# Kernel optimization log

Hardware: AMD Instinct MI355X
Metric: run time of the kernel (lower is better)

The kernel has to match this reference:

```python
import jax, jax.numpy as jnp
import numpy as np

B, N, H, HEADS, F, L = 32, 256, 512, 8, 2048, 8
D = H // HEADS  # per-head dim
EPS = 1e-5


def _layernorm(x, scale, bias):
    mu = jnp.mean(x, axis=-1, keepdims=True)
    var = jnp.mean(jnp.square(x - mu), axis=-1, keepdims=True)
    return (x - mu) * jax.lax.rsqrt(var + EPS) * scale + bias


def setup_inputs() -> dict:
    key = jax.random.key(0)
    ks = jax.random.split(key, 12)
    s = 0.02
    inp = {
        "x": jax.random.normal(ks[0], (B, N, H), jnp.float32),
        "attn_bias": jax.random.normal(ks[1], (B, HEADS, N, N), jnp.float32),
        "ln1_s": jnp.ones((L, H), jnp.float32),
        "ln1_b": jnp.zeros((L, H), jnp.float32),
        "wq": s * jax.random.normal(ks[2], (L, H, H), jnp.float32),
        "bq": jnp.zeros((L, H), jnp.float32),
        "wk": s * jax.random.normal(ks[3], (L, H, H), jnp.float32),
        "bk": jnp.zeros((L, H), jnp.float32),
        "wv": s * jax.random.normal(ks[4], (L, H, H), jnp.float32),
        "bv": jnp.zeros((L, H), jnp.float32),
        "wo": s * jax.random.normal(ks[5], (L, H, H), jnp.float32),
        "bo": jnp.zeros((L, H), jnp.float32),
        "ln2_s": jnp.ones((L, H), jnp.float32),
        "ln2_b": jnp.zeros((L, H), jnp.float32),
        "w1": s * jax.random.normal(ks[6], (L, H, F), jnp.float32),
        "b1": jnp.zeros((L, F), jnp.float32),
        "w2": s * jax.random.normal(ks[7], (L, F, H), jnp.float32),
        "b2": jnp.zeros((L, H), jnp.float32),
    }
    return inp


def reference(x, attn_bias, ln1_s, ln1_b, wq, bq, wk, bk, wv, bv, wo, bo,
              ln2_s, ln2_b, w1, b1, w2, b2):
    scale = D ** (-0.5)
    for l in range(L):
        # --- self attention block ---
        y = _layernorm(x, ln1_s[l], ln1_b[l])
        q = (y @ wq[l] + bq[l]).reshape(B, N, HEADS, D) * scale
        k = (y @ wk[l] + bk[l]).reshape(B, N, HEADS, D)
        v = (y @ wv[l] + bv[l]).reshape(B, N, HEADS, D)
        scores = jnp.einsum("bqhd,bkhd->bhqk", q, k) + attn_bias
        probs = jax.nn.softmax(scores, axis=-1)
        ctx = jnp.einsum("bhqk,bkhd->bqhd", probs, v).reshape(B, N, H)
        x = x + ctx @ wo[l] + bo[l]
        # --- FFN block ---
        y = _layernorm(x, ln2_s[l], ln2_b[l])
        y = jax.nn.gelu(y @ w1[l] + b1[l], approximate=False)
        x = x + y @ w2[l] + b2[l]
    return x
```

## Files before the change

### kernel.cpp

```cpp
#include <hip/hip_runtime.h>
#include <hip/hip_bf16.h>
#include <math.h>

typedef __bf16 bf16;
typedef __bf16 bf16x8 __attribute__((ext_vector_type(8)));
typedef float  f32x4  __attribute__((ext_vector_type(4)));

#define DEV __device__ __forceinline__

DEV f32x4 mfma16(bf16x8 a, bf16x8 b, f32x4 c) {
    return __builtin_amdgcn_mfma_f32_16x16x32_bf16(a, b, c, 0, 0, 0);
}

template <int MODE>
__global__ __launch_bounds__(256, 2) void gemm_k(
    const bf16* __restrict__ A, const bf16* __restrict__ Bt,
    const float* __restrict__ bias, bf16* __restrict__ Cb,
    int K, int ldC)
{
    __shared__ bf16 As[128 * 32];
    __shared__ bf16 Bs[128 * 32];
    const int tid  = threadIdx.x;
    const int lane = tid & 63;
    const int w    = tid >> 6;
    const int wm   = w & 1, wn = w >> 1;
    const long tm  = (long)blockIdx.y * 128;
    const long tn  = (long)blockIdx.x * 128;

    f32x4 acc[4][4] = {};

    const int p0 = tid, p1 = tid + 256;
    const int r0 = p0 >> 2, c0 = (p0 & 3) * 8;
    const int r1 = p1 >> 2, c1 = (p1 & 3) * 8;
    const int s0 = r0 * 32 + (((p0 & 3) ^ ((r0 >> 1) & 3)) * 8);
    const int s1 = r1 * 32 + (((p1 & 3) ^ ((r1 >> 1) & 3)) * 8);
    const bf16* A0 = A + (tm + r0) * K + c0;
    const bf16* A1 = A + (tm + r1) * K + c1;
    const bf16* B0 = Bt + (tn + r0) * K + c0;
    const bf16* B1 = Bt + (tn + r1) * K + c1;

    int am[4], bn[4];
#pragma unroll
    for (int i = 0; i < 4; ++i) {
        int ra = wm * 64 + i * 16 + (lane & 15);
        am[i]  = ra * 32 + (((lane >> 4) ^ ((ra >> 1) & 3)) * 8);
        int rb = wn * 64 + i * 16 + (lane & 15);
        bn[i]  = rb * 32 + (((lane >> 4) ^ ((rb >> 1) & 3)) * 8);
    }

    uint4 va0 = *(const uint4*)A0;
    uint4 va1 = *(const uint4*)A1;
    uint4 vb0 = *(const uint4*)B0;
    uint4 vb1 = *(const uint4*)B1;

    for (int k0 = 0; k0 < K; k0 += 32) {
        __syncthreads();
        *(uint4*)&As[s0] = va0;
        *(uint4*)&As[s1] = va1;
        *(uint4*)&Bs[s0] = vb0;
        *(uint4*)&Bs[s1] = vb1;
        __syncthreads();
        if (k0 + 32 < K) {
            va0 = *(const uint4*)(A0 + k0 + 32);
            va1 = *(const uint4*)(A1 + k0 + 32);
            vb0 = *(const uint4*)(B0 + k0 + 32);
            vb1 = *(const uint4*)(B1 + k0 + 32);
        }
        bf16x8 a[4], b[4];
#pragma unroll
        for (int i = 0; i < 4; ++i) a[i] = *(const bf16x8*)&As[am[i]];
#pragma unroll
        for (int i = 0; i < 4; ++i) b[i] = *(const bf16x8*)&Bs[bn[i]];
#pragma unroll
        for (int mi = 0; mi < 4; ++mi)
#pragma unroll
            for (int ni = 0; ni < 4; ++ni)
                acc[mi][ni] = mfma16(a[mi], b[ni], acc[mi][ni]);
    }

#pragma unroll
    for (int mi = 0; mi < 4; ++mi) {
        const long rbase = tm + wm * 64 + mi * 16 + ((lane >> 4) << 2);
#pragma unroll
        for (int ni = 0; ni < 4; ++ni) {
            const long col = tn + wn * 64 + ni * 16 + (lane & 15);
            const float bv = bias[col];
#pragma unroll
            for (int r = 0; r < 4; ++r) {
                float v = acc[mi][ni][r] + bv;
                if constexpr (MODE == 1)
                    v = 0.5f * v * (1.0f + erff(v * 0.70710678118654752f));
                Cb[(rbase + r) * (long)ldC + col] = (bf16)v;
            }
        }
    }
}

__global__ __launch_bounds__(256, 2) void gemm_dk(
    const bf16* __restrict__ A, const bf16* __restrict__ Bt,
    bf16* __restrict__ D, int K, int Ks)
{
    __shared__ bf16 As[128 * 32];
    __shared__ bf16 Bs[128 * 32];
    const int tid  = threadIdx.x;
    const int lane = tid & 63;
    const int w    = tid >> 6;
    const int wm   = w & 1, wn = w >> 1;
    const long tm  = (long)blockIdx.y * 128;
    const long tn  = (long)blockIdx.x * 128;
    const int kbase = blockIdx.z * Ks;

    f32x4 acc[4][4] = {};

    const int p0 = tid, p1 = tid + 256;
    const int r0 = p0 >> 2, c0 = (p0 & 3) * 8;
    const int r1 = p1 >> 2, c1 = (p1 & 3) * 8;
    const int s0 = r0 * 32 + (((p0 & 3) ^ ((r0 >> 1) & 3)) * 8);
    const int s1 = r1 * 32 + (((p1 & 3) ^ ((r1 >> 1) & 3)) * 8);
    const bf16* A0 = A + (tm + r0) * K + kbase + c0;
    const bf16* A1 = A + (tm + r1) * K + kbase + c1;
    const bf16* B0 = Bt + (tn + r0) * K + kbase + c0;
    const bf16* B1 = Bt + (tn + r1) * K + kbase + c1;

    int am[4], bn[4];
#pragma unroll
    for (int i = 0; i < 4; ++i) {
        int ra = wm * 64 + i * 16 + (lane & 15);
        am[i]  = ra * 32 + (((lane >> 4) ^ ((ra >> 1) & 3)) * 8);
        int rb = wn * 64 + i * 16 + (lane & 15);
        bn[i]  = rb * 32 + (((lane >> 4) ^ ((rb >> 1) & 3)) * 8);
    }

    uint4 va0 = *(const uint4*)A0;
    uint4 va1 = *(const uint4*)A1;
    uint4 vb0 = *(const uint4*)B0;
    uint4 vb1 = *(const uint4*)B1;

    for (int k0 = 0; k0 < Ks; k0 += 32) {
        __syncthreads();
        *(uint4*)&As[s0] = va0;
        *(uint4*)&As[s1] = va1;
        *(uint4*)&Bs[s0] = vb0;
        *(uint4*)&Bs[s1] = vb1;
        __syncthreads();
        if (k0 + 32 < Ks) {
            va0 = *(const uint4*)(A0 + k0 + 32);
            va1 = *(const uint4*)(A1 + k0 + 32);
            vb0 = *(const uint4*)(B0 + k0 + 32);
            vb1 = *(const uint4*)(B1 + k0 + 32);
        }
        bf16x8 a[4], b[4];
#pragma unroll
        for (int i = 0; i < 4; ++i) a[i] = *(const bf16x8*)&As[am[i]];
#pragma unroll
        for (int i = 0; i < 4; ++i) b[i] = *(const bf16x8*)&Bs[bn[i]];
#pragma unroll
        for (int mi = 0; mi < 4; ++mi)
#pragma unroll
            for (int ni = 0; ni < 4; ++ni)
                acc[mi][ni] = mfma16(a[mi], b[ni], acc[mi][ni]);
    }

    bf16* Dp = D + (long)blockIdx.z * 8192 * 512;
#pragma unroll
    for (int mi = 0; mi < 4; ++mi) {
        const long rbase = tm + wm * 64 + mi * 16 + ((lane >> 4) << 2);
#pragma unroll
        for (int ni = 0; ni < 4; ++ni) {
            const long col = tn + wn * 64 + ni * 16 + (lane & 15);
#pragma unroll
            for (int r = 0; r < 4; ++r)
                Dp[(rbase + r) * 512 + col] = (bf16)acc[mi][ni][r];
        }
    }
}

__global__ __launch_bounds__(256, 2) void attn_k(
    const bf16* __restrict__ qkv, const float* __restrict__ bias,
    bf16* __restrict__ ctx)
{
    __shared__ bf16 smem[256 * 72 + 32 * 264];
    bf16* Ks = smem;
    bf16* Vt = smem + 256 * 72;

    const int tid = threadIdx.x, lane = tid & 63, w = tid >> 6;
    const int qt = blockIdx.x & 3;
    const int h  = (blockIdx.x >> 2) & 7;
    const int b  = blockIdx.x >> 5;
    const long qkv_base = (long)b * 256 * 1536;

#pragma unroll
    for (int i = 0; i < 8; ++i) {
        int p = i * 256 + tid;
        int n = p >> 3, kk = (p & 7) * 8;
        uint4 v = *(const uint4*)(qkv + qkv_base + (long)n * 1536 + 512 + h * 64 + kk);
        *(uint4*)&Ks[n * 72 + kk] = v;
    }
    {
        int d = tid & 31, nb = tid >> 5;
#pragma unroll 4
        for (int i = 0; i < 32; ++i) {
            int n = nb + i * 8;
            Vt[d * 264 + n] = qkv[qkv_base + (long)n * 1536 + 1024 + h * 64 + d];
        }
    }

    const int qr0 = qt * 64 + w * 16;
    bf16x8 aq0, aq1;
    {
        const bf16* g = qkv + qkv_base + (long)(qr0 + (lane & 15)) * 1536 + h * 64 + ((lane >> 4) * 8);
        aq0 = *(const bf16x8*)g;
        aq1 = *(const bf16x8*)(g + 32);
    }
    __syncthreads();

    f32x4 s[16];
    const float* bb = bias + (((long)(b * 8 + h)) * 256 + qr0) * 256;
#pragma unroll
    for (int ct = 0; ct < 16; ++ct) {
        const int col = ct * 16 + (lane & 15);
        f32x4 c;
#pragma unroll
        for (int r = 0; r < 4; ++r)
            c[r] = bb[(long)((lane >> 4) * 4 + r) * 256 + col];
        bf16x8 k0 = *(const bf16x8*)&Ks[(ct * 16 + (lane & 15)) * 72 + ((lane >> 4) * 8)];
        bf16x8 k1 = *(const bf16x8*)&Ks[(ct * 16 + (lane & 15)) * 72 + 32 + ((lane >> 4) * 8)];
        c = mfma16(aq0, k0, c);
        c = mfma16(aq1, k1, c);
        s[ct] = c;
    }

    float m[4] = {-1e30f, -1e30f, -1e30f, -1e30f};
#pragma unroll
    for (int ct = 0; ct < 16; ++ct)
#pragma unroll
        for (int r = 0; r < 4; ++r) m[r] = fmaxf(m[r], s[ct][r]);
#pragma unroll
    for (int r = 0; r < 4; ++r)
#pragma unroll
        for (int off = 1; off < 16; off <<= 1)
            m[r] = fmaxf(m[r], __shfl_xor(m[r], off));
    float l[4] = {0.f, 0.f, 0.f, 0.f};
#pragma unroll
    for (int ct = 0; ct < 16; ++ct)
#pragma unroll
        for (int r = 0; r < 4; ++r) {
            float p = __expf(s[ct][r] - m[r]);
            s[ct][r] = p;
            l[r] += p;
        }
#pragma unroll
    for (int r = 0; r < 4; ++r) {
#pragma unroll
        for (int off = 1; off < 16; off <<= 1) l[r] += __shfl_xor(l[r], off);
        l[r] = 1.0f / l[r];
    }

    __syncthreads();
    bf16* P = Ks + w * (16 * 264);
#pragma unroll
    for (int ct = 0; ct < 16; ++ct)
#pragma unroll
        for (int r = 0; r < 4; ++r)
            P[(long)((lane >> 4) * 4 + r) * 264 + ct * 16 + (lane & 15)] = (bf16)s[ct][r];

    bf16x8 ap[8];
#pragma unroll
    for (int nk = 0; nk < 8; ++nk)
        ap[nk] = *(const bf16x8*)&P[(lane & 15) * 264 + nk * 32 + (lane >> 4) * 8];

    f32x4 o[4];
#pragma unroll
    for (int dt = 0; dt < 2; ++dt) {
        f32x4 c = {};
#pragma unroll
        for (int nk = 0; nk < 8; ++nk) {
            bf16x8 bv = *(const bf16x8*)&Vt[(dt * 16 + (lane & 15)) * 264 + nk * 32 + (lane >> 4) * 8];
            c = mfma16(ap[nk], bv, c);
        }
        o[dt] = c;
    }

    __syncthreads();
    {
        int d = tid & 31, nb = tid >> 5;
#pragma unroll 4
        for (int i = 0; i < 32; ++i) {
            int n = nb + i * 8;
            Vt[d * 264 + n] = qkv[qkv_base + (long)n * 1536 + 1024 + h * 64 + 32 + d];
        }
    }
    __syncthreads();
#pragma unroll
    for (int dt = 0; dt < 2; ++dt) {
        f32x4 c = {};
#pragma unroll
        for (int nk = 0; nk < 8; ++nk) {
            bf16x8 bv = *(const bf16x8*)&Vt[(dt * 16 + (lane & 15)) * 264 + nk * 32 + (lane >> 4) * 8];
            c = mfma16(ap[nk], bv, c);
        }
        o[2 + dt] = c;
    }

#pragma unroll
    for (int dt = 0; dt < 4; ++dt) {
        const int col = h * 64 + dt * 16 + (lane & 15);
#pragma unroll
        for (int r = 0; r < 4; ++r) {
            const long row = (long)b * 256 + qr0 + (lane >> 4) * 4 + r;
            ctx[row * 512 + col] = (bf16)(o[dt][r] * l[r]);
        }
    }
}

template <int NS>
__global__ __launch_bounds__(256) void ln_k(
    const float* __restrict__ x, float* __restrict__ xout,
    const bf16* __restrict__ d, const float* __restrict__ rbias,
    const float* __restrict__ sc, const float* __restrict__ bi,
    bf16* __restrict__ y)
{
    const int lane = threadIdx.x & 63;
    const long row = (long)blockIdx.x * 4 + (threadIdx.x >> 6);
    const float* xr = x + row * 512;
    float v[8];
    *(float4*)&v[0] = ((const float4*)xr)[lane * 2];
    *(float4*)&v[4] = ((const float4*)xr)[lane * 2 + 1];
    if constexpr (NS == 2) {
        bf16x8 d0 = *(const bf16x8*)&d[row * 512 + lane * 8];
        bf16x8 d1 = *(const bf16x8*)&d[(long)8192 * 512 + row * 512 + lane * 8];
        float b4[8];
        *(float4*)&b4[0] = ((const float4*)rbias)[lane * 2];
        *(float4*)&b4[4] = ((const float4*)rbias)[lane * 2 + 1];
#pragma unroll
        for (int j = 0; j < 8; ++j)
            v[j] += (float)d0[j] + (float)d1[j] + b4[j];
        float* xo = xout + row * 512;
        ((float4*)xo)[lane * 2]     = *(const float4*)&v[0];
        ((float4*)xo)[lane * 2 + 1] = *(const float4*)&v[4];
    }
    float sum = 0.f;
#pragma unroll
    for (int j = 0; j < 8; ++j) sum += v[j];
#pragma unroll
    for (int off = 1; off < 64; off <<= 1) sum += __shfl_xor(sum, off);
    const float mu = sum * (1.0f / 512.0f);
    float sq = 0.f;
#pragma unroll
    for (int j = 0; j < 8; ++j) { float dd = v[j] - mu; sq += dd * dd; }
#pragma unroll
    for (int off = 1; off < 64; off <<= 1) sq += __shfl_xor(sq, off);
    const float rs = rsqrtf(sq * (1.0f / 512.0f) + 1e-5f);
    bf16* yr = y + row * 512;
#pragma unroll
    for (int j = 0; j < 8; ++j) {
        int c = lane * 8 + j;
        yr[c] = (bf16)((v[j] - mu) * rs * sc[c] + bi[c]);
    }
}

__global__ __launch_bounds__(256) void addout_k(
    const float* __restrict__ x, const bf16* __restrict__ d,
    const float* __restrict__ rbias, float* __restrict__ out)
{
    const int lane = threadIdx.x & 63;
    const long row = (long)blockIdx.x * 4 + (threadIdx.x >> 6);
    float v[8];
    *(float4*)&v[0] = ((const float4*)(x + row * 512))[lane * 2];
    *(float4*)&v[4] = ((const float4*)(x + row * 512))[lane * 2 + 1];
    bf16x8 d0 = *(const bf16x8*)&d[row * 512 + lane * 8];
    bf16x8 d1 = *(const bf16x8*)&d[(long)8192 * 512 + row * 512 + lane * 8];
    float b4[8];
    *(float4*)&b4[0] = ((const float4*)rbias)[lane * 2];
    *(float4*)&b4[4] = ((const float4*)rbias)[lane * 2 + 1];
#pragma unroll
    for (int j = 0; j < 8; ++j)
        v[j] += (float)d0[j] + (float)d1[j] + b4[j];
    float* o = out + row * 512;
    ((float4*)o)[lane * 2]     = *(const float4*)&v[0];
    ((float4*)o)[lane * 2 + 1] = *(const float4*)&v[4];
}

__global__ __launch_bounds__(256) void transpose_k(
    const float* __restrict__ wq, const float* __restrict__ wk,
    const float* __restrict__ wv, const float* __restrict__ wo,
    const float* __restrict__ w1, const float* __restrict__ w2,
    bf16* __restrict__ qkvT, bf16* __restrict__ woT,
    bf16* __restrict__ w1T, bf16* __restrict__ w2T)
{
    __shared__ float tile[32][33];
    const int tid = threadIdx.x, tx = tid & 31, ty = tid >> 5;
    const int l = blockIdx.x / 3072;
    const int r = blockIdx.x % 3072;

    const float* In = nullptr;
    bf16* Out = nullptr;
    int Nd, tk, tn, rowOff = 0, ldO;
    float scale = 1.0f;
    if (r < 1024) {
        const int which = r >> 8, t = r & 255;
        tn = t >> 4; tk = t & 15; Nd = 512; ldO = 512;
        const long woff = (long)l * 512 * 512;
        if (which == 0)      { In = wq + woff; Out = qkvT + (long)l * 1536 * 512; rowOff = 0;    scale = 0.125f; }
        else if (which == 1) { In = wk + woff; Out = qkvT + (long)l * 1536 * 512; rowOff = 512;  }
        else if (which == 2) { In = wv + woff; Out = qkvT + (long)l * 1536 * 512; rowOff = 1024; }
        else                 { In = wo + woff; Out = woT + woff; }
    } else if (r < 2048) {
        const int t = r - 1024;
        tn = t >> 4; tk = t & 15; Nd = 2048; ldO = 512;
        In = w1 + (long)l * 512 * 2048; Out = w1T + (long)l * 2048 * 512;
    } else {
        const int t = r - 2048;
        tn = t & 15; tk = t >> 4; Nd = 512; ldO = 2048;
        In = w2 + (long)l * 2048 * 512; Out = w2T + (long)l * 512 * 2048;
    }
    const int gk = tk * 32, gn = tn * 32;
#pragma unroll
    for (int j = 0; j < 4; ++j) {
        int rr = ty + j * 8;
        tile[rr][tx] = In[(long)(gk + rr) * Nd + gn + tx] * scale;
    }
    __syncthreads();
#pragma unroll
    for (int j = 0; j < 4; ++j) {
        int rr = ty + j * 8;
        Out[(long)(rowOff + gn + rr) * ldO + gk + tx] = (bf16)tile[tx][rr];
    }
}

__global__ void biasq_k(const float* __restrict__ bq, const float* __restrict__ bk,
                        const float* __restrict__ bv, float* __restrict__ bqkv)
{
    int i = blockIdx.x * 256 + threadIdx.x;
    if (i >= 8 * 1536) return;
    int l = i / 1536, j = i % 1536;
    float v;
    if (j < 512)       v = bq[l * 512 + j] * 0.125f;
    else if (j < 1024) v = bk[l * 512 + j - 512];
    else               v = bv[l * 512 + j - 1024];
    bqkv[i] = v;
}

extern "C" void kernel_launch(void* const* d_in, const int* in_sizes, int n_in,
                              void* d_out, int out_size, void* d_ws, size_t ws_size,
                              hipStream_t stream)
{
    (void)in_sizes; (void)n_in; (void)out_size; (void)ws_size;
    const float* x    = (const float*)d_in[0];
    const float* ab   = (const float*)d_in[1];
    const float* ln1s = (const float*)d_in[2];
    const float* ln1b = (const float*)d_in[3];
    const float* wq   = (const float*)d_in[4];
    const float* bq   = (const float*)d_in[5];
    const float* wk   = (const float*)d_in[6];
    const float* bk   = (const float*)d_in[7];
    const float* wv   = (const float*)d_in[8];
    const float* bv   = (const float*)d_in[9];
    const float* wo   = (const float*)d_in[10];
    const float* bo   = (const float*)d_in[11];
    const float* ln2s = (const float*)d_in[12];
    const float* ln2b = (const float*)d_in[13];
    const float* w1   = (const float*)d_in[14];
    const float* b1   = (const float*)d_in[15];
    const float* w2   = (const float*)d_in[16];
    const float* b2   = (const float*)d_in[17];

    char* ws = (char*)d_ws;
    float* xf   = (float*)ws;
    bf16* y     = (bf16*)(ws + 16777216);
    bf16* ctx   = y;
    bf16* qkv   = (bf16*)(ws + 16777216 + 8388608);
    bf16* ffn   = qkv;
    bf16* dbuf  = (bf16*)(ws + 16777216 + 8388608 + 33554432);
    bf16* wqkvT = dbuf + (long)2 * 8192 * 512;
    bf16* woT   = wqkvT + (long)8 * 1536 * 512;
    bf16* w1T   = woT + (long)8 * 512 * 512;
    bf16* w2T   = w1T + (long)8 * 2048 * 512;
    float* bqkv = (float*)(w2T + (long)8 * 512 * 2048);

    hipMemcpyAsync(xf, x, (size_t)8192 * 512 * 4, hipMemcpyDeviceToDevice, stream);
    transpose_k<<<24576, 256, 0, stream>>>(wq, wk, wv, wo, w1, w2, wqkvT, woT, w1T, w2T);
    biasq_k<<<48, 256, 0, stream>>>(bq, bk, bv, bqkv);

    for (int l = 0; l < 8; ++l) {
        if (l == 0)
            ln_k<0><<<2048, 256, 0, stream>>>(xf, nullptr, nullptr, nullptr,
                                              ln1s, ln1b, y);
        else
            ln_k<2><<<2048, 256, 0, stream>>>(xf, xf, dbuf, b2 + (l - 1) * 512,
                                              ln1s + l * 512, ln1b + l * 512, y);
        gemm_k<0><<<dim3(12, 64), 256, 0, stream>>>(
            y, wqkvT + (long)l * 1536 * 512, bqkv + l * 1536, qkv, 512, 1536);
        attn_k<<<1024, 256, 0, stream>>>(qkv, ab, ctx);
        gemm_dk<<<dim3(4, 64, 2), 256, 0, stream>>>(
            ctx, woT + (long)l * 512 * 512, dbuf, 512, 256);
        ln_k<2><<<2048, 256, 0, stream>>>(xf, xf, dbuf, bo + l * 512,
                                          ln2s + l * 512, ln2b + l * 512, y);
        gemm_k<1><<<dim3(16, 64), 256, 0, stream>>>(
            y, w1T + (long)l * 2048 * 512, b1 + l * 2048, ffn, 512, 2048);
        gemm_dk<<<dim3(4, 64, 2), 256, 0, stream>>>(
            ffn, w2T + (long)l * 512 * 2048, dbuf, 2048, 1024);
    }
    addout_k<<<2048, 256, 0, stream>>>(xf, dbuf, b2 + 7 * 512, (float*)d_out);
}
```

Before: 1.365 ms.

## Load GEMM tiles directly to LDS and emit transposed V from QKV GEMM

```diff
diff --git a/kernel.cpp b/kernel.cpp
--- a/kernel.cpp
+++ b/kernel.cpp
@@ -4,6 +4,7 @@
 
 typedef __bf16 bf16;
 typedef __bf16 bf16x8 __attribute__((ext_vector_type(8)));
+typedef __bf16 bf16x4 __attribute__((ext_vector_type(4)));
 typedef float  f32x4  __attribute__((ext_vector_type(4)));
 
 #define DEV __device__ __forceinline__
@@ -12,11 +13,17 @@
     return __builtin_amdgcn_mfma_f32_16x16x32_bf16(a, b, c, 0, 0, 0);
 }
 
+DEV void gload16(const bf16* g, bf16* l) {
+    __builtin_amdgcn_global_load_lds(
+        (const __attribute__((address_space(1))) void*)g,
+        (__attribute__((address_space(3))) void*)l, 16, 0, 0);
+}
+
 template <int MODE>
-__global__ __launch_bounds__(256, 2) void gemm_k(
+__global__ __launch_bounds__(256, 3) void gemm_k(
     const bf16* __restrict__ A, const bf16* __restrict__ Bt,
     const float* __restrict__ bias, bf16* __restrict__ Cb,
-    int K, int ldC)
+    bf16* __restrict__ vt, int K, int ldC)
 {
     __shared__ bf16 As[128 * 32];
     __shared__ bf16 Bs[128 * 32];
@@ -29,15 +36,15 @@
 
     f32x4 acc[4][4] = {};
 
-    const int p0 = tid, p1 = tid + 256;
-    const int r0 = p0 >> 2, c0 = (p0 & 3) * 8;
-    const int r1 = p1 >> 2, c1 = (p1 & 3) * 8;
-    const int s0 = r0 * 32 + (((p0 & 3) ^ ((r0 >> 1) & 3)) * 8);
-    const int s1 = r1 * 32 + (((p1 & 3) ^ ((r1 >> 1) & 3)) * 8);
-    const bf16* A0 = A + (tm + r0) * K + c0;
-    const bf16* A1 = A + (tm + r1) * K + c1;
-    const bf16* B0 = Bt + (tn + r0) * K + c0;
-    const bf16* B1 = Bt + (tn + r1) * K + c1;
+    const int r0 = tid >> 2;
+    const int cc = ((tid & 3) ^ ((r0 >> 1) & 3)) * 8;
+    const bf16* Ag = A  + (tm + r0) * K + cc;
+    const bf16* Bg = Bt + (tn + r0) * K + cc;
+    const long rstep = (long)64 * K;
+    bf16* lA0 = &As[tid * 8];
+    bf16* lA1 = &As[(tid + 256) * 8];
+    bf16* lB0 = &Bs[tid * 8];
+    bf16* lB1 = &Bs[(tid + 256) * 8];
 
     int am[4], bn[4];
 #pragma unroll
@@ -48,24 +55,13 @@
         bn[i]  = rb * 32 + (((lane >> 4) ^ ((rb >> 1) & 3)) * 8);
     }
 
-    uint4 va0 = *(const uint4*)A0;
-    uint4 va1 = *(const uint4*)A1;
-    uint4 vb0 = *(const uint4*)B0;
-    uint4 vb1 = *(const uint4*)B1;
-
     for (int k0 = 0; k0 < K; k0 += 32) {
         __syncthreads();
-        *(uint4*)&As[s0] = va0;
-        *(uint4*)&As[s1] = va1;
-        *(uint4*)&Bs[s0] = vb0;
-        *(uint4*)&Bs[s1] = vb1;
+        gload16(Ag + k0,         lA0);
+        gload16(Ag + rstep + k0, lA1);
+        gload16(Bg + k0,         lB0);
+        gload16(Bg + rstep + k0, lB1);
         __syncthreads();
-        if (k0 + 32 < K) {
-            va0 = *(const uint4*)(A0 + k0 + 32);
-            va1 = *(const uint4*)(A1 + k0 + 32);
-            vb0 = *(const uint4*)(B0 + k0 + 32);
-            vb1 = *(const uint4*)(B1 + k0 + 32);
-        }
         bf16x8 a[4], b[4];
 #pragma unroll
         for (int i = 0; i < 4; ++i) a[i] = *(const bf16x8*)&As[am[i]];
@@ -85,18 +81,32 @@
         for (int ni = 0; ni < 4; ++ni) {
             const long col = tn + wn * 64 + ni * 16 + (lane & 15);
             const float bv = bias[col];
+            float v[4];
 #pragma unroll
             for (int r = 0; r < 4; ++r) {
-                float v = acc[mi][ni][r] + bv;
+                v[r] = acc[mi][ni][r] + bv;
                 if constexpr (MODE == 1)
-                    v = 0.5f * v * (1.0f + erff(v * 0.70710678118654752f));
-                Cb[(rbase + r) * (long)ldC + col] = (bf16)v;
+                    v[r] = 0.5f * v[r] * (1.0f + erff(v[r] * 0.70710678118654752f));
+            }
+            bool toV = false;
+            if constexpr (MODE == 2) toV = (col >= 1024);
+            if (toV) {
+                const int cv = (int)col - 1024;
+                const long bh = (rbase >> 8) * 8 + (cv >> 6);
+                bf16x4 pk;
+#pragma unroll
+                for (int r = 0; r < 4; ++r) pk[r] = (bf16)v[r];
+                *(bf16x4*)&vt[(bh * 64 + (cv & 63)) * 256 + (rbase & 255)] = pk;
+            } else {
+#pragma unroll
+                for (int r = 0; r < 4; ++r)
+                    Cb[(rbase + r) * (long)ldC + col] = (bf16)v[r];
             }
         }
     }
 }
 
-__global__ __launch_bounds__(256, 2) void gemm_dk(
+__global__ __launch_bounds__(256, 3) void gemm_dk(
     const bf16* __restrict__ A, const bf16* __restrict__ Bt,
     bf16* __restrict__ D, int K, int Ks)
 {
@@ -112,15 +122,15 @@
 
     f32x4 acc[4][4] = {};
 
-    const int p0 = tid, p1 = tid + 256;
-    const int r0 = p0 >> 2, c0 = (p0 & 3) * 8;
-    const int r1 = p1 >> 2, c1 = (p1 & 3) * 8;
-    const int s0 = r0 * 32 + (((p0 & 3) ^ ((r0 >> 1) & 3)) * 8);
-    const int s1 = r1 * 32 + (((p1 & 3) ^ ((r1 >> 1) & 3)) * 8);
-    const bf16* A0 = A + (tm + r0) * K + kbase + c0;
-    const bf16* A1 = A + (tm + r1) * K + kbase + c1;
-    const bf16* B0 = Bt + (tn + r0) * K + kbase + c0;
-    const bf16* B1 = Bt + (tn + r1) * K + kbase + c1;
+    const int r0 = tid >> 2;
+    const int cc = ((tid & 3) ^ ((r0 >> 1) & 3)) * 8;
+    const bf16* Ag = A  + (tm + r0) * K + kbase + cc;
+    const bf16* Bg = Bt + (tn + r0) * K + kbase + cc;
+    const long rstep = (long)64 * K;
+    bf16* lA0 = &As[tid * 8];
+    bf16* lA1 = &As[(tid + 256) * 8];
+    bf16* lB0 = &Bs[tid * 8];
+    bf16* lB1 = &Bs[(tid + 256) * 8];
 
     int am[4], bn[4];
 #pragma unroll
@@ -131,24 +141,13 @@
         bn[i]  = rb * 32 + (((lane >> 4) ^ ((rb >> 1) & 3)) * 8);
     }
 
-    uint4 va0 = *(const uint4*)A0;
-    uint4 va1 = *(const uint4*)A1;
-    uint4 vb0 = *(const uint4*)B0;
-    uint4 vb1 = *(const uint4*)B1;
-
     for (int k0 = 0; k0 < Ks; k0 += 32) {
         __syncthreads();
-        *(uint4*)&As[s0] = va0;
-        *(uint4*)&As[s1] = va1;
-        *(uint4*)&Bs[s0] = vb0;
-        *(uint4*)&Bs[s1] = vb1;
+        gload16(Ag + k0,         lA0);
+        gload16(Ag + rstep + k0, lA1);
+        gload16(Bg + k0,         lB0);
+        gload16(Bg + rstep + k0, lB1);
         __syncthreads();
-        if (k0 + 32 < Ks) {
-            va0 = *(const uint4*)(A0 + k0 + 32);
-            va1 = *(const uint4*)(A1 + k0 + 32);
-            vb0 = *(const uint4*)(B0 + k0 + 32);
-            vb1 = *(const uint4*)(B1 + k0 + 32);
-        }
         bf16x8 a[4], b[4];
 #pragma unroll
         for (int i = 0; i < 4; ++i) a[i] = *(const bf16x8*)&As[am[i]];
@@ -175,13 +174,12 @@
     }
 }
 
-__global__ __launch_bounds__(256, 2) void attn_k(
-    const bf16* __restrict__ qkv, const float* __restrict__ bias,
-    bf16* __restrict__ ctx)
-{
-    __shared__ bf16 smem[256 * 72 + 32 * 264];
+__global__ __launch_bounds__(256, 4) void attn_k(
+    const bf16* __restrict__ qkv, const bf16* __restrict__ vt,
+    const float* __restrict__ bias, bf16* __restrict__ ctx)
+{
+    __shared__ bf16 smem[256 * 72];
     bf16* Ks = smem;
-    bf16* Vt = smem + 256 * 72;
 
     const int tid = threadIdx.x, lane = tid & 63, w = tid >> 6;
     const int qt = blockIdx.x & 3;
@@ -195,14 +193,6 @@
         int n = p >> 3, kk = (p & 7) * 8;
         uint4 v = *(const uint4*)(qkv + qkv_base + (long)n * 1536 + 512 + h * 64 + kk);
         *(uint4*)&Ks[n * 72 + kk] = v;
-    }
-    {
-        int d = tid & 31, nb = tid >> 5;
-#pragma unroll 4
-        for (int i = 0; i < 32; ++i) {
-            int n = nb + i * 8;
-            Vt[d * 264 + n] = qkv[qkv_base + (long)n * 1536 + 1024 + h * 64 + d];
-        }
     }
 
     const int qr0 = qt * 64 + w * 16;
@@ -257,7 +247,7 @@
     }
 
     __syncthreads();
-    bf16* P = Ks + w * (16 * 264);
+    bf16* P = smem + w * (16 * 264);
 #pragma unroll
     for (int ct = 0; ct < 16; ++ct)
 #pragma unroll
@@ -269,37 +259,17 @@
     for (int nk = 0; nk < 8; ++nk)
         ap[nk] = *(const bf16x8*)&P[(lane & 15) * 264 + nk * 32 + (lane >> 4) * 8];
 
+    const bf16* vg = vt + (long)(b * 8 + h) * 64 * 256;
     f32x4 o[4];
 #pragma unroll
-    for (int dt = 0; dt < 2; ++dt) {
+    for (int dt = 0; dt < 4; ++dt) {
         f32x4 c = {};
 #pragma unroll
         for (int nk = 0; nk < 8; ++nk) {
-            bf16x8 bv = *(const bf16x8*)&Vt[(dt * 16 + (lane & 15)) * 264 + nk * 32 + (lane >> 4) * 8];
+            bf16x8 bv = *(const bf16x8*)&vg[(dt * 16 + (lane & 15)) * 256 + nk * 32 + (lane >> 4) * 8];
             c = mfma16(ap[nk], bv, c);
         }
         o[dt] = c;
-    }
-
-    __syncthreads();
-    {
-        int d = tid & 31, nb = tid >> 5;
-#pragma unroll 4
-        for (int i = 0; i < 32; ++i) {
-            int n = nb + i * 8;
-            Vt[d * 264 + n] = qkv[qkv_base + (long)n * 1536 + 1024 + h * 64 + 32 + d];
-        }
-    }
-    __syncthreads();
-#pragma unroll
-    for (int dt = 0; dt < 2; ++dt) {
-        f32x4 c = {};
-#pragma unroll
-        for (int nk = 0; nk < 8; ++nk) {
-            bf16x8 bv = *(const bf16x8*)&Vt[(dt * 16 + (lane & 15)) * 264 + nk * 32 + (lane >> 4) * 8];
-            c = mfma16(ap[nk], bv, c);
-        }
-        o[2 + dt] = c;
     }
 
 #pragma unroll
@@ -471,6 +441,7 @@
     bf16* ctx   = y;
     bf16* qkv   = (bf16*)(ws + 16777216 + 8388608);
     bf16* ffn   = qkv;
+    bf16* vt    = qkv + (long)8192 * 1536;
     bf16* dbuf  = (bf16*)(ws + 16777216 + 8388608 + 33554432);
     bf16* wqkvT = dbuf + (long)2 * 8192 * 512;
     bf16* woT   = wqkvT + (long)8 * 1536 * 512;
@@ -489,15 +460,15 @@
         else
             ln_k<2><<<2048, 256, 0, stream>>>(xf, xf, dbuf, b2 + (l - 1) * 512,
                                               ln1s + l * 512, ln1b + l * 512, y);
-        gemm_k<0><<<dim3(12, 64), 256, 0, stream>>>(
-            y, wqkvT + (long)l * 1536 * 512, bqkv + l * 1536, qkv, 512, 1536);
-        attn_k<<<1024, 256, 0, stream>>>(qkv, ab, ctx);
+        gemm_k<2><<<dim3(12, 64), 256, 0, stream>>>(
+            y, wqkvT + (long)l * 1536 * 512, bqkv + l * 1536, qkv, vt, 512, 1536);
+        attn_k<<<1024, 256, 0, stream>>>(qkv, vt, ab, ctx);
         gemm_dk<<<dim3(4, 64, 2), 256, 0, stream>>>(
             ctx, woT + (long)l * 512 * 512, dbuf, 512, 256);
         ln_k<2><<<2048, 256, 0, stream>>>(xf, xf, dbuf, bo + l * 512,
                                           ln2s + l * 512, ln2b + l * 512, y);
         gemm_k<1><<<dim3(16, 64), 256, 0, stream>>>(
-            y, w1T + (long)l * 2048 * 512, b1 + l * 2048, ffn, 512, 2048);
+            y, w1T + (long)l * 2048 * 512, b1 + l * 2048, ffn, nullptr, 512, 2048);
         gemm_dk<<<dim3(4, 64, 2), 256, 0, stream>>>(
             ffn, w2T + (long)l * 512 * 2048, dbuf, 2048, 1024);
     }
```

After: 1.388 ms. About the same (+1.7%).
